# Optimization experiments

Measured on AMD Instinct MI355X. Metric: run time of the kernel, lower is better.

Reference implementation:

```python
import jax, jax.numpy as jnp
import numpy as np

B, N, F, P, E, T = 8, 10000, 8, 12, 160000, 64
C = 32  # A3TGCN2 out_channels fixed to 32 in the module


def setup_inputs() -> dict:
    key = jax.random.key(0)
    ks = jax.random.split(key, 20)
    x = jax.random.normal(ks[0], (B, N, F, P), jnp.float32)
    edge_index = jax.random.randint(ks[1], (2, E), 0, N, dtype=jnp.int64)
    edge_weight = jax.random.uniform(ks[2], (E,), jnp.float32)

    def g(k, shape):
        return jax.random.normal(k, shape, jnp.float32) * 0.05

    return dict(
        x=x, edge_index=edge_index, edge_weight=edge_weight,
        Wz=g(ks[3], (F, C)), bz=g(ks[4], (C,)),
        Wr=g(ks[5], (F, C)), br=g(ks[6], (C,)),
        Wh=g(ks[7], (F, C)), bh=g(ks[8], (C,)),
        Lz_w=g(ks[9], (2 * C, C)), Lz_b=g(ks[10], (C,)),
        Lr_w=g(ks[11], (2 * C, C)), Lr_b=g(ks[12], (C,)),
        Lh_w=g(ks[13], (2 * C, C)), Lh_b=g(ks[14], (C,)),
        att=g(ks[15], (P,)),
        lin1_w=g(ks[16], (C, P)), lin1_b=g(ks[17], (P,)),
        lin2_w=g(ks[18], (N, T)), lin2_b=g(ks[19], (T,)),
    )


def _gcn_norm(edge_index, edge_weight, n):
    # GCNConv default: add self-loops (weight 1) + symmetric normalization
    row, col = edge_index[0], edge_index[1]
    loop = jnp.arange(n)
    row = jnp.concatenate([row, loop])
    col = jnp.concatenate([col, loop])
    w = jnp.concatenate([edge_weight, jnp.ones((n,), edge_weight.dtype)])
    deg = jax.ops.segment_sum(w, col, num_segments=n)
    dis = jnp.where(deg > 0, jax.lax.rsqrt(jnp.where(deg > 0, deg, 1.0)), 0.0)
    return row, col, dis[row] * w * dis[col]


def _gcn_conv(X, W, b, row, col, norm, n):
    XW = X @ W                                   # [B,N,C]
    msg = XW[:, row, :] * norm[None, :, None]    # gather over source nodes
    out = jnp.zeros((X.shape[0], n, W.shape[1]), X.dtype).at[:, col, :].add(msg)
    return out + b


def reference(x, edge_index, edge_weight, Wz, bz, Wr, br, Wh, bh,
              Lz_w, Lz_b, Lr_w, Lr_b, Lh_w, Lh_b, att,
              lin1_w, lin1_b, lin2_w, lin2_b):
    b_, n, _, periods = x.shape
    row, col, norm = _gcn_norm(edge_index, edge_weight, n)
    probs = jax.nn.softmax(att)
    # A3TGCN2 passes H=None to the TGCN cell at every period -> hidden state
    # is zeros for every period (faithful to library implementation).
    H0 = jnp.zeros((b_, n, Lz_w.shape[1]), x.dtype)
    H_accum = jnp.zeros_like(H0)
    for p in range(periods):
        Xp = x[:, :, :, p]                       # [B,N,F]
        Z = jax.nn.sigmoid(
            jnp.concatenate([_gcn_conv(Xp, Wz, bz, row, col, norm, n), H0], axis=2) @ Lz_w + Lz_b)
        R = jax.nn.sigmoid(
            jnp.concatenate([_gcn_conv(Xp, Wr, br, row, col, norm, n), H0], axis=2) @ Lr_w + Lr_b)
        Ht = jnp.tanh(
            jnp.concatenate([_gcn_conv(Xp, Wh, bh, row, col, norm, n), H0 * R], axis=2) @ Lh_w + Lh_b)
        H = Z * H0 + (1.0 - Z) * Ht
        H_accum = H_accum + probs[p] * H
    h = jax.nn.relu(H_accum)                     # [B,N,32]
    h = h @ lin1_w + lin1_b                      # [B,N,P]
    h = jnp.swapaxes(h, 2, 1)                    # [B,P,N]
    h = h @ lin2_w + lin2_b                      # [B,P,T]
    return jnp.swapaxes(h, 2, 1)                 # [B,T,P]
```

## Files before the change

kernel.cpp:

```cpp
#include <hip/hip_runtime.h>
#include <stdint.h>

#define NN 10000
#define NB 8
#define NP 12
#define NT 64
#define NC 32
#define BCAP 64
#define FCN 80
#define FCH 125
#define XB 3750

typedef float v2f __attribute__((ext_vector_type(2)));

__device__ __forceinline__ v2f up2(unsigned u) {
    v2f r;
    r.x = __uint_as_float(u << 16);
    r.y = __uint_as_float(u & 0xffff0000u);
    return r;
}
__device__ __forceinline__ v2f sp(float v) { v2f r; r.x = v; r.y = v; return r; }

__global__ __launch_bounds__(1024) void k_zero(int* __restrict__ p) {
    p[blockIdx.x * 1024 + threadIdx.x] = 0;
}

__global__ __launch_bounds__(256) void k_prep(
    const float* __restrict__ x,
    const int* __restrict__ rowp, const int* __restrict__ colp, const float* __restrict__ ew,
    const float* __restrict__ Wz, const float* __restrict__ bz,
    const float* __restrict__ Wh, const float* __restrict__ bh,
    const float* __restrict__ Lzw, const float* __restrict__ Lzb,
    const float* __restrict__ Lhw, const float* __restrict__ Lhb,
    const float* __restrict__ att,
    float* __restrict__ sm, float* __restrict__ deg, int* __restrict__ count,
    uint2* __restrict__ bucket, unsigned short* __restrict__ xh,
    int E, int EB) {
    const int blk = blockIdx.x, tid = threadIdx.x;
    if (blk < XB) {
        const int s = blk * 256 + tid;
        const int n = s / 96, r = s - n * 96;
        const int b = r / 12, q = r - b * 12;
        const float* px = x + (size_t)b * 960000 + n * 96 + q * 8;
        const float4 f0 = *(const float4*)px;
        const float4 f1 = *(const float4*)(px + 4);
        unsigned u0, u1, u2, u3;
        asm("v_cvt_pk_bf16_f32 %0, %1, %2" : "=v"(u0) : "v"(f0.x), "v"(f0.y));
        asm("v_cvt_pk_bf16_f32 %0, %1, %2" : "=v"(u1) : "v"(f0.z), "v"(f0.w));
        asm("v_cvt_pk_bf16_f32 %0, %1, %2" : "=v"(u2) : "v"(f1.x), "v"(f1.y));
        asm("v_cvt_pk_bf16_f32 %0, %1, %2" : "=v"(u3) : "v"(f1.z), "v"(f1.w));
        *(uint4*)(xh + (size_t)s * 8) = make_uint4(u0, u1, u2, u3);
    } else if (blk < XB + EB) {
        const int e = (blk - XB) * 256 + tid;
        if (e < E) {
            const int c = colp[e];
            const float w = ew[e];
            atomicAdd(&deg[c], w);
            const int slot = atomicAdd(&count[c], 1);
            if (slot < BCAP) bucket[slot * NN + c] = make_uint2((unsigned)rowp[e], __float_as_uint(w));
        }
    } else {
        const int t = tid, f = t >> 5, c = t & 31;
        float mz = 0.f, mh = 0.f;
        for (int j = 0; j < NC; ++j) {
            mz += Wz[f * NC + j] * Lzw[j * NC + c];
            mh += Wh[f * NC + j] * Lhw[j * NC + c];
        }
        sm[16 + 2 * t]     = mz;
        sm[16 + 2 * t + 1] = mh;
        if (t < NC) {
            float cz = Lzb[t], ch = Lhb[t];
            for (int j = 0; j < NC; ++j) {
                cz += bz[j] * Lzw[j * NC + t];
                ch += bh[j] * Lhw[j * NC + t];
            }
            sm[528 + 2 * t]     = cz;
            sm[528 + 2 * t + 1] = ch;
        }
        if (t == 0) {
            float m = -1e30f;
            for (int p = 0; p < NP; ++p) m = fmaxf(m, att[p]);
            float e[NP]; float s = 0.f;
            for (int p = 0; p < NP; ++p) { e[p] = __expf(att[p] - m); s += e[p]; }
            for (int p = 0; p < NP; ++p) sm[p] = e[p] / s;
        }
    }
}

#define ACCP(U0, U1, U2, VW)                                          \
    A[0] = __builtin_elementwise_fma(up2(U0.x), VW, A[0]);            \
    A[1] = __builtin_elementwise_fma(up2(U0.y), VW, A[1]);            \
    A[2] = __builtin_elementwise_fma(up2(U1.x), VW, A[2]);            \
    A[3] = __builtin_elementwise_fma(up2(U1.y), VW, A[3]);            \
    A[4] = __builtin_elementwise_fma(up2(U2.x), VW, A[4]);            \
    A[5] = __builtin_elementwise_fma(up2(U2.y), VW, A[5])

template<int PART>
__global__ __launch_bounds__(256) void k_main(
    const unsigned short* __restrict__ xh, const float* __restrict__ deg,
    const int* __restrict__ count, const uint2* __restrict__ bucket,
    const float* __restrict__ sm,
    const float* __restrict__ l1w, const float* __restrict__ l1b,
    float* __restrict__ h1t) {
    __shared__ float sY[4][800];
    __shared__ float sHA[4][264];
    __shared__ uint2 sE[4][64];

    const int tid = threadIdx.x;
    const int wv = tid >> 6, l = tid & 63;
    const int n = PART * 5000 + blockIdx.x * 4 + wv;

    const char* xbase = (const char*)xh;
    const unsigned loff = (unsigned)l * 24u;
    const float dn = rsqrtf(deg[n] + 1.0f);
    v2f A[6];
    {
        const v2f vsn = sp(dn * dn);
        const char* p0 = xbase + ((unsigned)n * 1536u + loff);
        const uint2 u0 = *(const uint2*)p0;
        const uint2 u1 = *(const uint2*)(p0 + 8);
        const uint2 u2 = *(const uint2*)(p0 + 16);
        A[0] = up2(u0.x) * vsn; A[1] = up2(u0.y) * vsn;
        A[2] = up2(u1.x) * vsn; A[3] = up2(u1.y) * vsn;
        A[4] = up2(u2.x) * vsn; A[5] = up2(u2.y) * vsn;
    }
    const int cnt = min(count[n], BCAP);
    uint2* sEw = &sE[wv][0];
    {
        uint2 ent = make_uint2(0u, 0u);
        if (l < cnt) {
            const uint2 e = bucket[l * NN + n];
            const float w = __uint_as_float(e.y);
            const float nrm = rsqrtf(deg[e.x] + 1.0f) * w * dn;
            ent = make_uint2(e.x * 1536u, __float_as_uint(nrm));
        }
        sEw[l] = ent;
    }
    const int m4 = (cnt + 3) & ~3;
    for (int q = 0; q < m4; q += 4) {
        const uint2 e0 = sEw[q + 0], e1 = sEw[q + 1], e2 = sEw[q + 2], e3 = sEw[q + 3];
        const char* pA = xbase + (e0.x + loff);
        const char* pB = xbase + (e1.x + loff);
        const char* pC = xbase + (e2.x + loff);
        const char* pD = xbase + (e3.x + loff);
        const uint2 A0 = *(const uint2*)pA, A1 = *(const uint2*)(pA + 8), A2 = *(const uint2*)(pA + 16);
        const uint2 B0 = *(const uint2*)pB, B1 = *(const uint2*)(pB + 8), B2 = *(const uint2*)(pB + 16);
        const uint2 C0 = *(const uint2*)pC, C1 = *(const uint2*)(pC + 8), C2 = *(const uint2*)(pC + 16);
        const uint2 D0 = *(const uint2*)pD, D1 = *(const uint2*)(pD + 8), D2 = *(const uint2*)(pD + 16);
        const v2f w0 = sp(__uint_as_float(e0.y)), w1 = sp(__uint_as_float(e1.y));
        const v2f w2 = sp(__uint_as_float(e2.y)), w3 = sp(__uint_as_float(e3.y));
        ACCP(A0, A1, A2, w0);
        ACCP(B0, B1, B2, w1);
        ACCP(C0, C1, C2, w2);
        ACCP(D0, D1, D2, w3);
    }
    {
        float* yp = &sY[wv][(l >> 3) * 100 + (l & 7) * 12];
        *(float4*)yp       = make_float4(A[0].x, A[0].y, A[1].x, A[1].y);
        *(float4*)(yp + 4) = make_float4(A[2].x, A[2].y, A[3].x, A[3].y);
        *(float4*)(yp + 8) = make_float4(A[4].x, A[4].y, A[5].x, A[5].y);
    }

    const int c = l & 31;
    const float2* __restrict__ smzh = (const float2*)(sm + 16);
    const float2* __restrict__ sczh = (const float2*)(sm + 528);
    v2f m8[8];
    #pragma unroll
    for (int f = 0; f < 8; ++f) { const float2 t2 = smzh[f * 32 + c]; v2f v; v.x = t2.x; v.y = t2.y; m8[f] = v; }
    v2f czh;
    { const float2 t2 = sczh[c]; czh.x = t2.x; czh.y = t2.y; }
    float pr[12];
    #pragma unroll
    for (int p = 0; p < 12; ++p) pr[p] = sm[p];

    #pragma unroll
    for (int t4 = 0; t4 < 4; ++t4) {
        const int b = t4 * 2 + (l >> 5);
        const float* yb = &sY[wv][b * 100];
        v2f zh[12];
        #pragma unroll
        for (int p = 0; p < 12; ++p) zh[p] = czh;
        #pragma unroll
        for (int f = 0; f < 8; ++f) {
            const float4 y0 = *(const float4*)(yb + f * 12);
            const float4 y1 = *(const float4*)(yb + f * 12 + 4);
            const float4 y2 = *(const float4*)(yb + f * 12 + 8);
            const v2f mm = m8[f];
            zh[0]  = __builtin_elementwise_fma(sp(y0.x), mm, zh[0]);
            zh[1]  = __builtin_elementwise_fma(sp(y0.y), mm, zh[1]);
            zh[2]  = __builtin_elementwise_fma(sp(y0.z), mm, zh[2]);
            zh[3]  = __builtin_elementwise_fma(sp(y0.w), mm, zh[3]);
            zh[4]  = __builtin_elementwise_fma(sp(y1.x), mm, zh[4]);
            zh[5]  = __builtin_elementwise_fma(sp(y1.y), mm, zh[5]);
            zh[6]  = __builtin_elementwise_fma(sp(y1.z), mm, zh[6]);
            zh[7]  = __builtin_elementwise_fma(sp(y1.w), mm, zh[7]);
            zh[8]  = __builtin_elementwise_fma(sp(y2.x), mm, zh[8]);
            zh[9]  = __builtin_elementwise_fma(sp(y2.y), mm, zh[9]);
            zh[10] = __builtin_elementwise_fma(sp(y2.z), mm, zh[10]);
            zh[11] = __builtin_elementwise_fma(sp(y2.w), mm, zh[11]);
        }
        float hacc = 0.f;
        #pragma unroll
        for (int p = 0; p < 12; ++p) {
            const float u = __expf(-zh[p].x);
            const float v = __expf(2.f * zh[p].y);
            const float num = u * (v - 1.f);
            const float den = fmaf(u, v, u) + (v + 1.f);
            hacc = fmaf(pr[p] * num, __builtin_amdgcn_rcpf(den), hacc);
        }
        sHA[wv][b * 33 + c] = fmaxf(hacc, 0.f);
    }

    {
        const int r = l;
        const int bb = r / 12, p = r - bb * 12;
        float s = l1b[p];
        #pragma unroll
        for (int cc = 0; cc < 32; ++cc) s = fmaf(sHA[wv][bb * 33 + cc], l1w[cc * 12 + p], s);
        h1t[n * 96 + r] = s;
    }
    if (l < 32) {
        const int r = l + 64;
        const int bb = r / 12, p = r - bb * 12;
        float s = l1b[p];
        #pragma unroll
        for (int cc = 0; cc < 32; ++cc) s = fmaf(sHA[wv][bb * 33 + cc], l1w[cc * 12 + p], s);
        h1t[n * 96 + r] = s;
    }
}

__global__ __launch_bounds__(256) void k_final(const float* __restrict__ h1t, const float* __restrict__ W2,
                                               float* __restrict__ partial) {
    __shared__ float sh1[96 * FCN];
    const int tid = threadIdx.x;
    const int n0 = blockIdx.x * FCN;

    for (int idx = tid; idx < 96 * FCN; idx += 256) {
        const int nn = idx / 96, i = idx - nn * 96;
        sh1[i * FCN + nn] = h1t[(n0 + nn) * 96 + i];
    }
    __syncthreads();

    const int t = tid & 63, w = tid >> 6;
    const float* sh = &sh1[w * 24 * FCN];
    float acc[24];
    #pragma unroll
    for (int j = 0; j < 24; ++j) acc[j] = 0.f;

    for (int nn = 0; nn < FCN; nn += 4) {
        const float w20 = W2[(n0 + nn + 0) * NT + t];
        const float w21 = W2[(n0 + nn + 1) * NT + t];
        const float w22 = W2[(n0 + nn + 2) * NT + t];
        const float w23 = W2[(n0 + nn + 3) * NT + t];
        #pragma unroll
        for (int j = 0; j < 24; ++j) {
            const float4 hv = *(const float4*)&sh[j * FCN + nn];
            acc[j] = fmaf(hv.x, w20, fmaf(hv.y, w21, fmaf(hv.z, w22, fmaf(hv.w, w23, acc[j]))));
        }
    }

    float* pp = partial + blockIdx.x * 6144 + w * 24 * 64 + t;
    #pragma unroll
    for (int j = 0; j < 24; ++j) pp[j * 64] = acc[j];
}

__global__ __launch_bounds__(256) void k_red(const float* __restrict__ partial, const float* __restrict__ l2b,
                                             float* __restrict__ out) {
    __shared__ float red[4][64];
    const int i = blockIdx.x;
    const int t = threadIdx.x & 63, g = threadIdx.x >> 6;
    float s = 0.f;
    for (int c = g; c < FCH; c += 4)
        s += partial[c * 6144 + i * 64 + t];
    red[g][t] = s;
    __syncthreads();
    if (g == 0) {
        const float v = red[0][t] + red[1][t] + red[2][t] + red[3][t] + l2b[t];
        const int b = i / 12, p = i - b * 12;
        out[b * 768 + t * 12 + p] = v;
    }
}

extern "C" void kernel_launch(void* const* d_in, const int* in_sizes, int n_in,
                              void* d_out, int out_size, void* d_ws, size_t ws_size,
                              hipStream_t stream) {
    const float* x    = (const float*)d_in[0];
    const int*   eidx = (const int*)d_in[1];
    const float* ew   = (const float*)d_in[2];
    const float* Wz   = (const float*)d_in[3];
    const float* bz   = (const float*)d_in[4];
    const float* Wh   = (const float*)d_in[7];
    const float* bh   = (const float*)d_in[8];
    const float* Lzw  = (const float*)d_in[9];
    const float* Lzb  = (const float*)d_in[10];
    const float* Lhw  = (const float*)d_in[13];
    const float* Lhb  = (const float*)d_in[14];
    const float* att  = (const float*)d_in[15];
    const float* l1w  = (const float*)d_in[16];
    const float* l1b  = (const float*)d_in[17];
    const float* W2   = (const float*)d_in[18];
    const float* l2b  = (const float*)d_in[19];
    float* out = (float*)d_out;
    const int E = in_sizes[2];
    const int EB = (E + 255) / 256;

    float* deg    = (float*)d_ws;
    int*   count  = (int*)(deg + 10240);
    uint2* bucket = (uint2*)(count + 10240);
    float* sm     = (float*)(bucket + NN * BCAP);
    float* h1t    = sm + 1024;
    unsigned short* xh = (unsigned short*)(h1t + NN * 96);
    float* partial = (float*)(xh + (size_t)NN * 768);

    const int* rowp = eidx;
    const int* colp = eidx + E;

    hipLaunchKernelGGL(k_zero, dim3(20), dim3(1024), 0, stream, (int*)d_ws);
    hipLaunchKernelGGL(k_prep, dim3(XB + EB + 1), dim3(256), 0, stream,
                       x, rowp, colp, ew, Wz, bz, Wh, bh, Lzw, Lzb, Lhw, Lhb, att,
                       sm, deg, count, bucket, xh, E, EB);
    k_main<0><<<dim3(1250), dim3(256), 0, stream>>>(xh, deg, count, bucket, sm, l1w, l1b, h1t);
    k_main<1><<<dim3(1250), dim3(256), 0, stream>>>(xh, deg, count, bucket, sm, l1w, l1b, h1t);
    hipLaunchKernelGGL(k_final, dim3(FCH), dim3(256), 0, stream, h1t, W2, partial);
    hipLaunchKernelGGL(k_red, dim3(96), dim3(256), 0, stream, partial, l2b, out);
}
```

Before: 126.3 us.

## Use batch-major bf16 node layout and map eight nodes per wave in aggregation

Stores the bf16 feature copy batch-major with padded node rows, so each gathered neighbour row is 192 bytes from one batch instead of 1536 bytes covering all batches. The main kernel now runs one block per (batch, 32-node chunk), with eight lanes per node, and loads edges in rounds of eight up to the wave's largest degree. The two half-launches are merged into a single launch. The aim is a smaller per-batch gather working set that stays in cache and fewer idle lanes per edge. The cost is that edge-bucket reads and normalization are now repeated for every batch, and nodes with few edges wait on the highest-degree node in their wave.

```diff
diff --git a/kernel.cpp b/kernel.cpp
--- a/kernel.cpp
+++ b/kernel.cpp
@@ -2,6 +2,7 @@
 #include <stdint.h>
 
 #define NN 10000
+#define NNP 10016
 #define NB 8
 #define NP 12
 #define NT 64
@@ -39,8 +40,8 @@
     const int blk = blockIdx.x, tid = threadIdx.x;
     if (blk < XB) {
         const int s = blk * 256 + tid;
-        const int n = s / 96, r = s - n * 96;
-        const int b = r / 12, q = r - b * 12;
+        const int b = s / 120000, rem = s - b * 120000;
+        const int n = rem / 12, q = rem - n * 12;
         const float* px = x + (size_t)b * 960000 + n * 96 + q * 8;
         const float4 f0 = *(const float4*)px;
         const float4 f1 = *(const float4*)(px + 4);
@@ -49,7 +50,7 @@
         asm("v_cvt_pk_bf16_f32 %0, %1, %2" : "=v"(u1) : "v"(f0.z), "v"(f0.w));
         asm("v_cvt_pk_bf16_f32 %0, %1, %2" : "=v"(u2) : "v"(f1.x), "v"(f1.y));
         asm("v_cvt_pk_bf16_f32 %0, %1, %2" : "=v"(u3) : "v"(f1.z), "v"(f1.w));
-        *(uint4*)(xh + (size_t)s * 8) = make_uint4(u0, u1, u2, u3);
+        *(uint4*)(xh + ((size_t)(b * NNP + n) * 12 + q) * 8) = make_uint4(u0, u1, u2, u3);
     } else if (blk < XB + EB) {
         const int e = (blk - XB) * 256 + tid;
         if (e < E) {
@@ -87,15 +88,6 @@
     }
 }
 
-#define ACCP(U0, U1, U2, VW)                                          \
-    A[0] = __builtin_elementwise_fma(up2(U0.x), VW, A[0]);            \
-    A[1] = __builtin_elementwise_fma(up2(U0.y), VW, A[1]);            \
-    A[2] = __builtin_elementwise_fma(up2(U1.x), VW, A[2]);            \
-    A[3] = __builtin_elementwise_fma(up2(U1.y), VW, A[3]);            \
-    A[4] = __builtin_elementwise_fma(up2(U2.x), VW, A[4]);            \
-    A[5] = __builtin_elementwise_fma(up2(U2.y), VW, A[5])
-
-template<int PART>
 __global__ __launch_bounds__(256) void k_main(
     const unsigned short* __restrict__ xh, const float* __restrict__ deg,
     const int* __restrict__ count, const uint2* __restrict__ bucket,
@@ -108,15 +100,18 @@
 
     const int tid = threadIdx.x;
     const int wv = tid >> 6, l = tid & 63;
-    const int n = PART * 5000 + blockIdx.x * 4 + wv;
-
-    const char* xbase = (const char*)xh;
-    const unsigned loff = (unsigned)l * 24u;
+    const int b = blockIdx.x & 7;
+    const int chunk = blockIdx.x >> 3;
+    const int g = l >> 3, j8 = l & 7;
+    const int n = chunk * 32 + wv * 8 + g;
+    const char* xb = (const char*)(xh + (size_t)b * NNP * 96);
+
+    const int cnt = min(count[n], BCAP);
     const float dn = rsqrtf(deg[n] + 1.0f);
     v2f A[6];
     {
         const v2f vsn = sp(dn * dn);
-        const char* p0 = xbase + ((unsigned)n * 1536u + loff);
+        const char* p0 = xb + ((unsigned)n * 192u + (unsigned)j8 * 24u);
         const uint2 u0 = *(const uint2*)p0;
         const uint2 u1 = *(const uint2*)(p0 + 8);
         const uint2 u2 = *(const uint2*)(p0 + 16);
@@ -124,38 +119,39 @@
         A[2] = up2(u1.x) * vsn; A[3] = up2(u1.y) * vsn;
         A[4] = up2(u2.x) * vsn; A[5] = up2(u2.y) * vsn;
     }
-    const int cnt = min(count[n], BCAP);
+
+    int mcnt = cnt;
+    #pragma unroll
+    for (int off = 1; off < 64; off <<= 1) mcnt = max(mcnt, __shfl_xor(mcnt, off));
+
     uint2* sEw = &sE[wv][0];
+    for (int base = 0; base < mcnt; base += 8) {
+        uint2 ent = make_uint2(0u, 0u);
+        const int e = base + j8;
+        if (e < cnt) {
+            const uint2 be = bucket[e * NN + n];
+            const float nrm = rsqrtf(deg[be.x] + 1.0f) * __uint_as_float(be.y) * dn;
+            ent = make_uint2(be.x * 192u, __float_as_uint(nrm));
+        }
+        sEw[l] = ent;
+        #pragma unroll
+        for (int j = 0; j < 8; ++j) {
+            const uint2 e2 = sEw[g * 8 + j];
+            const v2f w = sp(__uint_as_float(e2.y));
+            const char* p = xb + (e2.x + (unsigned)j8 * 24u);
+            const uint2 u0 = *(const uint2*)p;
+            const uint2 u1 = *(const uint2*)(p + 8);
+            const uint2 u2 = *(const uint2*)(p + 16);
+            A[0] = __builtin_elementwise_fma(up2(u0.x), w, A[0]);
+            A[1] = __builtin_elementwise_fma(up2(u0.y), w, A[1]);
+            A[2] = __builtin_elementwise_fma(up2(u1.x), w, A[2]);
+            A[3] = __builtin_elementwise_fma(up2(u1.y), w, A[3]);
+            A[4] = __builtin_elementwise_fma(up2(u2.x), w, A[4]);
+            A[5] = __builtin_elementwise_fma(up2(u2.y), w, A[5]);
+        }
+    }
     {
-        uint2 ent = make_uint2(0u, 0u);
-        if (l < cnt) {
-            const uint2 e = bucket[l * NN + n];
-            const float w = __uint_as_float(e.y);
-            const float nrm = rsqrtf(deg[e.x] + 1.0f) * w * dn;
-            ent = make_uint2(e.x * 1536u, __float_as_uint(nrm));
-        }
-        sEw[l] = ent;
-    }
-    const int m4 = (cnt + 3) & ~3;
-    for (int q = 0; q < m4; q += 4) {
-        const uint2 e0 = sEw[q + 0], e1 = sEw[q + 1], e2 = sEw[q + 2], e3 = sEw[q + 3];
-        const char* pA = xbase + (e0.x + loff);
-        const char* pB = xbase + (e1.x + loff);
-        const char* pC = xbase + (e2.x + loff);
-        const char* pD = xbase + (e3.x + loff);
-        const uint2 A0 = *(const uint2*)pA, A1 = *(const uint2*)(pA + 8), A2 = *(const uint2*)(pA + 16);
-        const uint2 B0 = *(const uint2*)pB, B1 = *(const uint2*)(pB + 8), B2 = *(const uint2*)(pB + 16);
-        const uint2 C0 = *(const uint2*)pC, C1 = *(const uint2*)(pC + 8), C2 = *(const uint2*)(pC + 16);
-        const uint2 D0 = *(const uint2*)pD, D1 = *(const uint2*)(pD + 8), D2 = *(const uint2*)(pD + 16);
-        const v2f w0 = sp(__uint_as_float(e0.y)), w1 = sp(__uint_as_float(e1.y));
-        const v2f w2 = sp(__uint_as_float(e2.y)), w3 = sp(__uint_as_float(e3.y));
-        ACCP(A0, A1, A2, w0);
-        ACCP(B0, B1, B2, w1);
-        ACCP(C0, C1, C2, w2);
-        ACCP(D0, D1, D2, w3);
-    }
-    {
-        float* yp = &sY[wv][(l >> 3) * 100 + (l & 7) * 12];
+        float* yp = &sY[wv][g * 100 + j8 * 12];
         *(float4*)yp       = make_float4(A[0].x, A[0].y, A[1].x, A[1].y);
         *(float4*)(yp + 4) = make_float4(A[2].x, A[2].y, A[3].x, A[3].y);
         *(float4*)(yp + 8) = make_float4(A[4].x, A[4].y, A[5].x, A[5].y);
@@ -175,8 +171,8 @@
 
     #pragma unroll
     for (int t4 = 0; t4 < 4; ++t4) {
-        const int b = t4 * 2 + (l >> 5);
-        const float* yb = &sY[wv][b * 100];
+        const int nd = t4 * 2 + (l >> 5);
+        const float* yb = &sY[wv][nd * 100];
         v2f zh[12];
         #pragma unroll
         for (int p = 0; p < 12; ++p) zh[p] = czh;
@@ -208,24 +204,28 @@
             const float den = fmaf(u, v, u) + (v + 1.f);
             hacc = fmaf(pr[p] * num, __builtin_amdgcn_rcpf(den), hacc);
         }
-        sHA[wv][b * 33 + c] = fmaxf(hacc, 0.f);
-    }
-
+        sHA[wv][nd * 33 + c] = fmaxf(hacc, 0.f);
+    }
+
+    const int n0w = chunk * 32 + wv * 8;
     {
-        const int r = l;
-        const int bb = r / 12, p = r - bb * 12;
+        const int nd = l / 12, p = l - nd * 12;
+        if (nd < 8) {
+            float s = l1b[p];
+            #pragma unroll
+            for (int cc = 0; cc < 32; ++cc) s = fmaf(sHA[wv][nd * 33 + cc], l1w[cc * 12 + p], s);
+            const int nn = n0w + nd;
+            if (nn < NN) h1t[nn * 96 + b * 12 + p] = s;
+        }
+    }
+    if (l < 32) {
+        const int task = l + 64;
+        const int nd = task / 12, p = task - nd * 12;
         float s = l1b[p];
         #pragma unroll
-        for (int cc = 0; cc < 32; ++cc) s = fmaf(sHA[wv][bb * 33 + cc], l1w[cc * 12 + p], s);
-        h1t[n * 96 + r] = s;
-    }
-    if (l < 32) {
-        const int r = l + 64;
-        const int bb = r / 12, p = r - bb * 12;
-        float s = l1b[p];
-        #pragma unroll
-        for (int cc = 0; cc < 32; ++cc) s = fmaf(sHA[wv][bb * 33 + cc], l1w[cc * 12 + p], s);
-        h1t[n * 96 + r] = s;
+        for (int cc = 0; cc < 32; ++cc) s = fmaf(sHA[wv][nd * 33 + cc], l1w[cc * 12 + p], s);
+        const int nn = n0w + nd;
+        if (nn < NN) h1t[nn * 96 + b * 12 + p] = s;
     }
 }
 
@@ -310,7 +310,7 @@
     float* sm     = (float*)(bucket + NN * BCAP);
     float* h1t    = sm + 1024;
     unsigned short* xh = (unsigned short*)(h1t + NN * 96);
-    float* partial = (float*)(xh + (size_t)NN * 768);
+    float* partial = (float*)(xh + (size_t)NB * NNP * 96);
 
     const int* rowp = eidx;
     const int* colp = eidx + E;
@@ -319,8 +319,8 @@
     hipLaunchKernelGGL(k_prep, dim3(XB + EB + 1), dim3(256), 0, stream,
                        x, rowp, colp, ew, Wz, bz, Wh, bh, Lzw, Lzb, Lhw, Lhb, att,
                        sm, deg, count, bucket, xh, E, EB);
-    k_main<0><<<dim3(1250), dim3(256), 0, stream>>>(xh, deg, count, bucket, sm, l1w, l1b, h1t);
-    k_main<1><<<dim3(1250), dim3(256), 0, stream>>>(xh, deg, count, bucket, sm, l1w, l1b, h1t);
+    hipLaunchKernelGGL(k_main, dim3(313 * 8), dim3(256), 0, stream,
+                       xh, deg, count, bucket, sm, l1w, l1b, h1t);
     hipLaunchKernelGGL(k_final, dim3(FCH), dim3(256), 0, stream, h1t, W2, partial);
     hipLaunchKernelGGL(k_red, dim3(96), dim3(256), 0, stream, partial, l2b, out);
 }
```

Result: faster. 112.4 us (-11.0%).
